# Kernel optimization log

Hardware: AMD Instinct MI355X
Metric: run time of the kernel (lower is better)

Reference implementation:

```python
import jax, jax.numpy as jnp
import numpy as np

IN_CAPS, IN_SIZE = 2401, 8
OUT_CAPS, OUT_SIZE = 8, 16
ROUTING_ITERS = 3


def squash(s, axis):
    mag_sq = jnp.sum(s * s, axis=axis, keepdims=True)
    mag = jnp.sqrt(mag_sq)
    return mag_sq / (1.0 + mag_sq) * (s / mag)


def setup_inputs() -> dict:
    key = jax.random.key(0)
    kx, kw = jax.random.split(key)
    B = 256
    x = jax.random.normal(kx, (B, IN_CAPS, IN_SIZE), dtype=jnp.float32)
    stdv = 1.0 / np.sqrt(IN_CAPS)
    W = jax.random.uniform(kw, (IN_CAPS, OUT_CAPS, OUT_SIZE, IN_SIZE),
                           dtype=jnp.float32, minval=-stdv, maxval=stdv)
    return {"x": x, "W": W}


def reference(x, W):
    # u_hat[b,i,o,c] = W[i,o,c,d] @ x[b,i,d]   -> [B, 2401, 8, 16]
    u_hat = jnp.einsum('iocd,bid->bioc', W, x)
    u_hat_det = jax.lax.stop_gradient(u_hat)

    b_ij = jnp.zeros((IN_CAPS, OUT_CAPS), dtype=x.dtype)
    v_j = None
    for it in range(ROUTING_ITERS):
        c_ij = jax.nn.softmax(b_ij, axis=1)  # softmax over out_capsules
        last = (it == ROUTING_ITERS - 1)
        u = u_hat if last else u_hat_det
        s_j = jnp.einsum('io,bioc->boc', c_ij, u)  # [B, 8, 16]
        v_j = squash(s_j, axis=-1)
        if not last:
            # agreement: mean over batch of <u_hat_i, v_j>
            a = jnp.einsum('bioc,boc->io', u_hat_det, v_j) / x.shape[0]
            b_ij = b_ij + a
    return v_j  # [B, 8, 16]
```

## Files before the change

kernel.cpp:

```cpp
#include <hip/hip_runtime.h>
#include <math.h>

#define IC     2401
#define BSZ    256
#define OC     8
#define CS     16
#define OCC    128
#define XROW   19208
#define KP     19264
#define KTILES 301
#define NI     64

typedef __attribute__((ext_vector_type(8))) short short8;
typedef __attribute__((ext_vector_type(4))) float f32x4;

__device__ __forceinline__ unsigned short f2bf(float f) {
    union { float f; unsigned u; } v; v.f = f;
    const unsigned r = v.u + 0x7FFF + ((v.u >> 16) & 1);
    return (unsigned short)(r >> 16);
}
__device__ __forceinline__ float bf2f(unsigned short h) {
    union { unsigned u; float f; } v; v.u = ((unsigned)h) << 16;
    return v.f;
}

__global__ __launch_bounds__(256)
void prep_kernel(const float* __restrict__ x, const float* __restrict__ W,
                 unsigned short* __restrict__ xT, unsigned short* __restrict__ xB,
                 unsigned short* __restrict__ Wbf, unsigned short* __restrict__ cwt)
{
    const int tid = threadIdx.x;
    if (blockIdx.x < 1204) {
        __shared__ float Ts[64 * 65];
        const int bg = blockIdx.x & 3;
        const int kt = blockIdx.x >> 2;
#pragma unroll
        for (int r = 0; r < 4; ++r) {
            const int flat = r * 256 + tid;
            const int b = flat >> 4, cq = flat & 15;
            const int col = kt * 64 + cq * 4;
            float4 v = make_float4(0.f, 0.f, 0.f, 0.f);
            if (col < XROW) v = *(const float4*)(x + (size_t)(bg * 64 + b) * XROW + col);
            *(float4*)&Ts[b * 65 + cq * 4] = v;
        }
        __syncthreads();
#pragma unroll
        for (int r = 0; r < 2; ++r) {
            const int flat = r * 256 + tid;
            const int rl = flat >> 3, bq = flat & 7;
            union { short8 v; unsigned short h[8]; } o;
#pragma unroll
            for (int j = 0; j < 8; ++j) o.h[j] = f2bf(Ts[(bq * 8 + j) * 65 + rl]);
            *(short8*)(xT + (size_t)(kt * 64 + rl) * 256 + bg * 64 + bq * 8) = o.v;
        }
#pragma unroll
        for (int r = 0; r < 2; ++r) {
            const int flat = r * 256 + tid;
            const int b = flat >> 3, g = flat & 7;
            union { short8 v; unsigned short h[8]; } o;
#pragma unroll
            for (int j = 0; j < 8; ++j) o.h[j] = f2bf(Ts[b * 65 + g * 8 + j]);
            *(short8*)(xB + (size_t)(bg * 64 + b) * KP + (size_t)kt * 64 + g * 8) = o.v;
        }
    } else {
        __shared__ float Ws[8 * 1032];
        const int i0 = (blockIdx.x - 1204) * 8;
#pragma unroll
        for (int r = 0; r < 8; ++r) {
            const int flat = r * 256 + tid;
            const int g = flat >> 8, rem = flat & 255;
            int gi = i0 + g; if (gi > 2400) gi = 2400;
            const float4 v = *(const float4*)(W + (size_t)gi * 1024 + rem * 4);
            *(float4*)&Ws[g * 1032 + rem * 4] = v;
        }
        __syncthreads();
#pragma unroll
        for (int r = 0; r < 4; ++r) {
            const int flat = r * 256 + tid;
            const int oc = flat >> 3, g = flat & 7;
            const int gi = i0 + g;
            union { short8 v; unsigned short h[8]; } w, c;
            if (gi <= 2400) {
                const float* wp = &Ws[g * 1032 + oc * 8];
#pragma unroll
                for (int j = 0; j < 8; ++j) {
                    w.h[j] = f2bf(wp[j]);
                    c.h[j] = f2bf(0.125f * wp[j]);
                }
            } else {
#pragma unroll
                for (int j = 0; j < 8; ++j) { w.h[j] = 0; c.h[j] = 0; }
            }
            *(short8*)(Wbf + (size_t)oc * KP + (size_t)gi * 8) = w.v;
            *(short8*)(cwt + (size_t)oc * KP + (size_t)gi * 8) = c.v;
        }
    }
}

__global__ __launch_bounds__(256, 2)
void s_gemm(const unsigned short* __restrict__ xB, const unsigned short* __restrict__ cwt,
            float* __restrict__ spart)
{
    __shared__ __align__(16) unsigned short Xs[64 * 64];
    __shared__ __align__(16) unsigned short Bs[128 * 64];
    const int tid = threadIdx.x;
    const int bg  = blockIdx.x, iy = blockIdx.y;
    const int b0  = bg * 64;
    const int ln  = tid & 63;
    const int mr  = ln & 15, qd = ln >> 4;
    const int mh  = (tid >> 6) & 1;
    const int nh  = tid >> 7;

    f32x4 acc[2][4];
#pragma unroll
    for (int a = 0; a < 2; ++a)
#pragma unroll
        for (int b = 0; b < 4; ++b) acc[a][b] = (f32x4){0.f, 0.f, 0.f, 0.f};

    for (int kt = iy; kt < KTILES; kt += NI) {
        __syncthreads();
#pragma unroll
        for (int r = 0; r < 2; ++r) {
            const int flat = r * 256 + tid;
            const int b = flat >> 3, col = flat & 7;
            const short8 v = *(const short8*)(xB + (size_t)(b0 + b) * KP + (size_t)(kt * 8 + col) * 8);
            *(short8*)&Xs[b * 64 + ((col ^ (b & 7)) * 8)] = v;
        }
#pragma unroll
        for (int r = 0; r < 4; ++r) {
            const int flat = r * 256 + tid;
            const int oc = flat >> 3, col = flat & 7;
            const short8 w = *(const short8*)(cwt + (size_t)oc * KP + (size_t)(kt * 8 + col) * 8);
            *(short8*)&Bs[oc * 64 + ((col ^ (oc & 7)) * 8)] = w;
        }
        __syncthreads();
#pragma unroll
        for (int kk = 0; kk < 2; ++kk) {
            const int csw = ((kk * 4 + qd) ^ (mr & 7)) * 8;
            const short8 a0 = *(const short8*)&Xs[(mh * 32 + mr) * 64 + csw];
            const short8 a1 = *(const short8*)&Xs[(mh * 32 + 16 + mr) * 64 + csw];
#pragma unroll
            for (int nt = 0; nt < 4; ++nt) {
                const short8 b = *(const short8*)&Bs[(nh * 64 + nt * 16 + mr) * 64 + csw];
                acc[0][nt] = __builtin_amdgcn_mfma_f32_16x16x32_bf16(a0, b, acc[0][nt], 0, 0, 0);
                acc[1][nt] = __builtin_amdgcn_mfma_f32_16x16x32_bf16(a1, b, acc[1][nt], 0, 0, 0);
            }
        }
    }

    float* op = spart + ((size_t)iy * BSZ + b0) * OCC;
#pragma unroll
    for (int mt = 0; mt < 2; ++mt)
#pragma unroll
        for (int nt = 0; nt < 4; ++nt)
#pragma unroll
            for (int r = 0; r < 4; ++r)
                op[(size_t)(mh * 32 + mt * 16 + qd * 4 + r) * OCC + nh * 64 + nt * 16 + mr]
                    = acc[mt][nt][r];
}

__global__ __launch_bounds__(256)
void squash_kernel(const float* __restrict__ spart, float* __restrict__ vout,
                   unsigned short* __restrict__ vT, int writeT)
{
    __shared__ float red[256];
    const int tid = threadIdx.x;
    const int r0  = blockIdx.x * 8;
    const int idx = tid & 127;
    const int k0  = tid >> 7;

    const float* base = spart + (size_t)r0 * 16 + idx;
    float acc = 0.0f;
#pragma unroll 8
    for (int k = k0; k < NI; k += 2) acc += base[(size_t)k * (BSZ * OCC)];
    red[tid] = acc;
    __syncthreads();

    if (tid < 128) {
        const float s = red[tid] + red[tid + 128];
        float ms = s * s;
        ms += __shfl_xor(ms, 1); ms += __shfl_xor(ms, 2);
        ms += __shfl_xor(ms, 4); ms += __shfl_xor(ms, 8);
        const float scale = sqrtf(ms) / (1.0f + ms);
        const float outv = s * scale;
        const int row = r0 + (tid >> 4);
        const int j   = tid & 15;
        if (writeT) {
            vT[(size_t)((row & 7) * 16 + j) * 256 + (row >> 3)] = f2bf(outv);
        } else {
            vout[(size_t)row * 16 + j] = outv;
        }
    }
}

template<bool FIRST>
__global__ __launch_bounds__(256, 2)
void a_gemm(const unsigned short* __restrict__ xT, const unsigned short* __restrict__ vT,
            const unsigned short* __restrict__ Wbf, float* __restrict__ bij,
            unsigned short* __restrict__ cwt)
{
    __shared__ __align__(16) char smraw[128 * 68 * 4];
    unsigned short* As = (unsigned short*)smraw;
    unsigned short* Bx = (unsigned short*)(smraw + 16384);
    float* Hs = (float*)smraw;

    const int tid = threadIdx.x;
    const int i0  = blockIdx.x * 8;
    const int ln  = tid & 63, wv = tid >> 6;
    const int mr  = ln & 15, qd = ln >> 4;

    f32x4 acc[2][4];
#pragma unroll
    for (int a = 0; a < 2; ++a)
#pragma unroll
        for (int b = 0; b < 4; ++b) acc[a][b] = (f32x4){0.f, 0.f, 0.f, 0.f};

    for (int bc = 0; bc < 4; ++bc) {
        __syncthreads();
#pragma unroll
        for (int r = 0; r < 4; ++r) {
            const int flat = r * 256 + tid;
            const int oc = flat >> 3, col = flat & 7;
            const short8 v = *(const short8*)(vT + (size_t)oc * 256 + bc * 64 + col * 8);
            *(short8*)&As[oc * 64 + ((col ^ (oc & 7)) * 8)] = v;
        }
#pragma unroll
        for (int r = 0; r < 2; ++r) {
            const int flat = r * 256 + tid;
            const int rw = flat >> 3, col = flat & 7;
            const short8 v = *(const short8*)(xT + (size_t)(i0 * 8 + rw) * 256 + bc * 64 + col * 8);
            *(short8*)&Bx[rw * 64 + ((col ^ (rw & 7)) * 8)] = v;
        }
        __syncthreads();
#pragma unroll
        for (int kk = 0; kk < 2; ++kk) {
            const int csw = ((kk * 4 + qd) ^ (mr & 7)) * 8;
#pragma unroll
            for (int nt = 0; nt < 4; ++nt) {
                const short8 b = *(const short8*)&Bx[(nt * 16 + mr) * 64 + csw];
#pragma unroll
                for (int mt = 0; mt < 2; ++mt) {
                    const short8 a = *(const short8*)&As[((wv * 2 + mt) * 16 + mr) * 64 + csw];
                    acc[mt][nt] = __builtin_amdgcn_mfma_f32_16x16x32_bf16(a, b, acc[mt][nt], 0, 0, 0);
                }
            }
        }
    }

    __syncthreads();
#pragma unroll
    for (int mt = 0; mt < 2; ++mt)
#pragma unroll
        for (int nt = 0; nt < 4; ++nt)
#pragma unroll
            for (int r = 0; r < 4; ++r)
                Hs[((wv * 2 + mt) * 16 + qd * 4 + r) * 68 + nt * 16 + mr] = acc[mt][nt][r];
    __syncthreads();

    const int ch = tid & 3, oo = (tid >> 2) & 7, il = tid >> 5;
    const int ival = i0 + il;
    const int gi = (ival < IC) ? ival : IC - 1;
    const unsigned short* Wt = Wbf + (size_t)(oo * 16 + ch * 4) * KP + (size_t)gi * 8;

    float wreg[4][8];
#pragma unroll
    for (int c = 0; c < 4; ++c) {
        union { short8 v; unsigned short h[8]; } uw;
        uw.v = *(const short8*)(Wt + (size_t)c * KP);
#pragma unroll
        for (int j = 0; j < 8; ++j) wreg[c][j] = bf2f(uw.h[j]);
    }
    float p = 0.0f;
#pragma unroll
    for (int c = 0; c < 4; ++c) {
        const float* hr = &Hs[(oo * 16 + ch * 4 + c) * 68 + il * 8];
        const float4 h0 = *(const float4*)hr;
        const float4 h1 = *(const float4*)(hr + 4);
        p = fmaf(wreg[c][0], h0.x, p); p = fmaf(wreg[c][1], h0.y, p);
        p = fmaf(wreg[c][2], h0.z, p); p = fmaf(wreg[c][3], h0.w, p);
        p = fmaf(wreg[c][4], h1.x, p); p = fmaf(wreg[c][5], h1.y, p);
        p = fmaf(wreg[c][6], h1.z, p); p = fmaf(wreg[c][7], h1.w, p);
    }
    p += __shfl_xor(p, 1); p += __shfl_xor(p, 2);
    const float anew = p * (1.0f / 256.0f);
    float bv = anew;
    if (!FIRST) bv += bij[gi * 8 + oo];
    float mx = bv;
    mx = fmaxf(mx, __shfl_xor(mx, 4));
    mx = fmaxf(mx, __shfl_xor(mx, 8));
    mx = fmaxf(mx, __shfl_xor(mx, 16));
    const float e = expf(bv - mx);
    float ss = e;
    ss += __shfl_xor(ss, 4); ss += __shfl_xor(ss, 8); ss += __shfl_xor(ss, 16);
    float cv = e / ss;
    if (ival >= IC) cv = 0.0f;
    if (ch == 0 && ival < IC) bij[ival * 8 + oo] = bv;
#pragma unroll
    for (int c = 0; c < 4; ++c) {
        union { short8 v; unsigned short h[8]; } o;
#pragma unroll
        for (int j = 0; j < 8; ++j) o.h[j] = f2bf(cv * wreg[c][j]);
        *(short8*)(cwt + (size_t)(oo * 16 + ch * 4 + c) * KP + (size_t)ival * 8) = o.v;
    }
}

extern "C" void kernel_launch(void* const* d_in, const int* in_sizes, int n_in,
                              void* d_out, int out_size, void* d_ws, size_t ws_size,
                              hipStream_t stream)
{
    const float* x = (const float*)d_in[0];
    const float* W = (const float*)d_in[1];
    float* out = (float*)d_out;

    char* p = (char*)d_ws;
    float*          spart = (float*)p;          p += (size_t)NI * BSZ * OCC * 4;
    unsigned short* xT    = (unsigned short*)p; p += (size_t)KP * 256 * 2;
    unsigned short* xB    = (unsigned short*)p; p += (size_t)256 * KP * 2;
    unsigned short* Wbf   = (unsigned short*)p; p += (size_t)128 * KP * 2;
    unsigned short* cwt   = (unsigned short*)p; p += (size_t)128 * KP * 2;
    unsigned short* vT    = (unsigned short*)p; p += (size_t)128 * 256 * 2;
    float*          bij   = (float*)p;

    const dim3 sgrid(4, NI);

    prep_kernel<<<1505, 256, 0, stream>>>(x, W, xT, xB, Wbf, cwt);

    s_gemm<<<sgrid, 256, 0, stream>>>(xB, cwt, spart);
    squash_kernel<<<256, 256, 0, stream>>>(spart, nullptr, vT, 1);
    a_gemm<true><<<KTILES, 256, 0, stream>>>(xT, vT, Wbf, bij, cwt);
    s_gemm<<<sgrid, 256, 0, stream>>>(xB, cwt, spart);
    squash_kernel<<<256, 256, 0, stream>>>(spart, nullptr, vT, 1);
    a_gemm<false><<<KTILES, 256, 0, stream>>>(xT, vT, Wbf, bij, cwt);
    s_gemm<<<sgrid, 256, 0, stream>>>(xB, cwt, spart);
    squash_kernel<<<256, 256, 0, stream>>>(spart, out, vT, 0);
}
```

Baseline: 142.4 us.

## Fuse routing iterations into one persistent cooperative kernel with grid syncs

Replaces the eight separate s_gemm/squash/a_gemm launches with a single cooperative kernel of 256 blocks that runs all routing phases and separates them with grid-wide syncs. This is meant to remove per-launch overhead and the gaps between dependent kernels. In exchange, the a_gemm phase now runs with 256 blocks looping over 301 tiles, so a few blocks do two tiles. Occupancy also drops to one block per CU, and every grid.sync has its own cost. If the cooperative launch fails, the code falls back to separate launches.

Result: slower. 380.9 us (+167.4%).

```diff
diff --git a/kernel.cpp b/kernel.cpp
--- a/kernel.cpp
+++ b/kernel.cpp
@@ -1,5 +1,8 @@
 #include <hip/hip_runtime.h>
+#include <hip/hip_cooperative_groups.h>
 #include <math.h>
+
+namespace cg = cooperative_groups;
 
 #define IC     2401
 #define BSZ    256
@@ -97,19 +100,18 @@
     }
 }
 
-__global__ __launch_bounds__(256, 2)
-void s_gemm(const unsigned short* __restrict__ xB, const unsigned short* __restrict__ cwt,
-            float* __restrict__ spart)
-{
-    __shared__ __align__(16) unsigned short Xs[64 * 64];
-    __shared__ __align__(16) unsigned short Bs[128 * 64];
-    const int tid = threadIdx.x;
-    const int bg  = blockIdx.x, iy = blockIdx.y;
-    const int b0  = bg * 64;
-    const int ln  = tid & 63;
-    const int mr  = ln & 15, qd = ln >> 4;
-    const int mh  = (tid >> 6) & 1;
-    const int nh  = tid >> 7;
+__device__ __forceinline__ void s_phase(char* smraw, const int tid, const int bid,
+        const unsigned short* __restrict__ xB, const unsigned short* __restrict__ cwt,
+        float* __restrict__ spart)
+{
+    unsigned short* Xs = (unsigned short*)smraw;
+    unsigned short* Bs = (unsigned short*)(smraw + 8192);
+    const int bg = bid & 3, iy = bid >> 2;
+    const int b0 = bg * 64;
+    const int ln = tid & 63;
+    const int mr = ln & 15, qd = ln >> 4;
+    const int mh = (tid >> 6) & 1;
+    const int nh = tid >> 7;
 
     f32x4 acc[2][4];
 #pragma unroll
@@ -159,13 +161,11 @@
                     = acc[mt][nt][r];
 }
 
-__global__ __launch_bounds__(256)
-void squash_kernel(const float* __restrict__ spart, float* __restrict__ vout,
-                   unsigned short* __restrict__ vT, int writeT)
-{
-    __shared__ float red[256];
-    const int tid = threadIdx.x;
-    const int r0  = blockIdx.x * 8;
+__device__ __forceinline__ void q_phase(char* smraw, const int tid, const int bid, const int writeT,
+        const float* __restrict__ spart, float* __restrict__ vout, unsigned short* __restrict__ vT)
+{
+    float* red = (float*)smraw;
+    const int r0  = bid * 8;
     const int idx = tid & 127;
     const int k0  = tid >> 7;
 
@@ -193,19 +193,16 @@
     }
 }
 
-template<bool FIRST>
-__global__ __launch_bounds__(256, 2)
-void a_gemm(const unsigned short* __restrict__ xT, const unsigned short* __restrict__ vT,
-            const unsigned short* __restrict__ Wbf, float* __restrict__ bij,
-            unsigned short* __restrict__ cwt)
-{
-    __shared__ __align__(16) char smraw[128 * 68 * 4];
+__device__ __forceinline__ void a_phase(char* smraw, const int tid, const int t, const int first,
+        const unsigned short* __restrict__ xT, const unsigned short* __restrict__ vT,
+        const unsigned short* __restrict__ Wbf, float* __restrict__ bij,
+        unsigned short* __restrict__ cwt)
+{
     unsigned short* As = (unsigned short*)smraw;
     unsigned short* Bx = (unsigned short*)(smraw + 16384);
     float* Hs = (float*)smraw;
 
-    const int tid = threadIdx.x;
-    const int i0  = blockIdx.x * 8;
+    const int i0  = t * 8;
     const int ln  = tid & 63, wv = tid >> 6;
     const int mr  = ln & 15, qd = ln >> 4;
 
@@ -284,7 +281,7 @@
     p += __shfl_xor(p, 1); p += __shfl_xor(p, 2);
     const float anew = p * (1.0f / 256.0f);
     float bv = anew;
-    if (!FIRST) bv += bij[gi * 8 + oo];
+    if (!first) bv += bij[gi * 8 + oo];
     float mx = bv;
     mx = fmaxf(mx, __shfl_xor(mx, 4));
     mx = fmaxf(mx, __shfl_xor(mx, 8));
@@ -304,6 +301,60 @@
     }
 }
 
+__global__ __launch_bounds__(256, 1)
+void routing_kernel(const unsigned short* __restrict__ xT,
+                    const unsigned short* __restrict__ xB,
+                    const unsigned short* __restrict__ Wbf,
+                    unsigned short* __restrict__ cwt,
+                    float* __restrict__ spart,
+                    unsigned short* __restrict__ vT,
+                    float* __restrict__ bij,
+                    float* __restrict__ out)
+{
+    cg::grid_group grid = cg::this_grid();
+    __shared__ __align__(16) char sm[128 * 68 * 4];
+    const int tid = threadIdx.x;
+    const int bid = blockIdx.x;
+
+#pragma unroll 1
+    for (int iter = 0; iter < 3; ++iter) {
+        s_phase(sm, tid, bid, xB, cwt, spart);
+        grid.sync();
+        q_phase(sm, tid, bid, (iter < 2) ? 1 : 0, spart, out, vT);
+        if (iter == 2) return;
+        grid.sync();
+        for (int t = bid; t < KTILES; t += 256)
+            a_phase(sm, tid, t, (iter == 0) ? 1 : 0, xT, vT, Wbf, bij, cwt);
+        grid.sync();
+    }
+}
+
+__global__ __launch_bounds__(256, 2)
+void s_gemm_k(const unsigned short* __restrict__ xB, const unsigned short* __restrict__ cwt,
+              float* __restrict__ spart)
+{
+    __shared__ __align__(16) char sm[24576];
+    s_phase(sm, threadIdx.x, blockIdx.x, xB, cwt, spart);
+}
+
+__global__ __launch_bounds__(256)
+void squash_k(const float* __restrict__ spart, float* __restrict__ vout,
+              unsigned short* __restrict__ vT, int writeT)
+{
+    __shared__ __align__(16) char sm[1024];
+    q_phase(sm, threadIdx.x, blockIdx.x, writeT, spart, vout, vT);
+}
+
+__global__ __launch_bounds__(256, 2)
+void a_gemm_k(const unsigned short* __restrict__ xT, const unsigned short* __restrict__ vT,
+              const unsigned short* __restrict__ Wbf, float* __restrict__ bij,
+              unsigned short* __restrict__ cwt, int first)
+{
+    __shared__ __align__(16) char sm[34816];
+    for (int t = blockIdx.x; t < KTILES; t += gridDim.x)
+        a_phase(sm, threadIdx.x, t, first, xT, vT, Wbf, bij, cwt);
+}
+
 extern "C" void kernel_launch(void* const* d_in, const int* in_sizes, int n_in,
                               void* d_out, int out_size, void* d_ws, size_t ws_size,
                               hipStream_t stream)
@@ -321,16 +372,20 @@
     unsigned short* vT    = (unsigned short*)p; p += (size_t)128 * 256 * 2;
     float*          bij   = (float*)p;
 
-    const dim3 sgrid(4, NI);
-
     prep_kernel<<<1505, 256, 0, stream>>>(x, W, xT, xB, Wbf, cwt);
 
-    s_gemm<<<sgrid, 256, 0, stream>>>(xB, cwt, spart);
-    squash_kernel<<<256, 256, 0, stream>>>(spart, nullptr, vT, 1);
-    a_gemm<true><<<KTILES, 256, 0, stream>>>(xT, vT, Wbf, bij, cwt);
-    s_gemm<<<sgrid, 256, 0, stream>>>(xB, cwt, spart);
-    squash_kernel<<<256, 256, 0, stream>>>(spart, nullptr, vT, 1);
-    a_gemm<false><<<KTILES, 256, 0, stream>>>(xT, vT, Wbf, bij, cwt);
-    s_gemm<<<sgrid, 256, 0, stream>>>(xB, cwt, spart);
-    squash_kernel<<<256, 256, 0, stream>>>(spart, out, vT, 0);
-}
+    void* kargs[] = { (void*)&xT, (void*)&xB, (void*)&Wbf, (void*)&cwt,
+                      (void*)&spart, (void*)&vT, (void*)&bij, (void*)&out };
+    hipError_t err = hipLaunchCooperativeKernel((void*)routing_kernel,
+                                                dim3(256), dim3(256), kargs, 0, stream);
+    if (err != hipSuccess) {
+        s_gemm_k<<<256, 256, 0, stream>>>(xB, cwt, spart);
+        squash_k<<<256, 256, 0, stream>>>(spart, nullptr, vT, 1);
+        a_gemm_k<<<256, 256, 0, stream>>>(xT, vT, Wbf, bij, cwt, 1);
+        s_gemm_k<<<256, 256, 0, stream>>>(xB, cwt, spart);
+        squash_k<<<256, 256, 0, stream>>>(spart, nullptr, vT, 1);
+        a_gemm_k<<<256, 256, 0, stream>>>(xT, vT, Wbf, bij, cwt, 0);
+        s_gemm_k<<<256, 256, 0, stream>>>(xB, cwt, spart);
+        squash_k<<<256, 256, 0, stream>>>(spart, out, vT, 0);
+    }
+}
```

## Register-prefetch next K tile in both MFMA GEMMs and double split-K partitions

Applied to the files above, without the earlier changes.

Both MFMA GEMM kernels now load the next tile's global data into registers before computing on the current shared-memory tile. This overlaps global-load latency with the MFMA work. The split-K factor NI also doubles from 64 to 128, giving more blocks for parallelism. The cost is more partial sums for the squash/reduce kernel to read and some extra register pressure.

Result: no change. 141.3 us (-0.8%).

```diff
diff --git a/kernel.cpp b/kernel.cpp
--- a/kernel.cpp
+++ b/kernel.cpp
@@ -9,7 +9,7 @@
 #define XROW   19208
 #define KP     19264
 #define KTILES 301
-#define NI     64
+#define NI     128
 
 typedef __attribute__((ext_vector_type(8))) short short8;
 typedef __attribute__((ext_vector_type(4))) float f32x4;
@@ -117,21 +117,30 @@
 #pragma unroll
         for (int b = 0; b < 4; ++b) acc[a][b] = (f32x4){0.f, 0.f, 0.f, 0.f};
 
-    for (int kt = iy; kt < KTILES; kt += NI) {
-        __syncthreads();
-#pragma unroll
-        for (int r = 0; r < 2; ++r) {
-            const int flat = r * 256 + tid;
-            const int b = flat >> 3, col = flat & 7;
-            const short8 v = *(const short8*)(xB + (size_t)(b0 + b) * KP + (size_t)(kt * 8 + col) * 8);
-            *(short8*)&Xs[b * 64 + ((col ^ (b & 7)) * 8)] = v;
-        }
-#pragma unroll
-        for (int r = 0; r < 4; ++r) {
-            const int flat = r * 256 + tid;
-            const int oc = flat >> 3, col = flat & 7;
-            const short8 w = *(const short8*)(cwt + (size_t)oc * KP + (size_t)(kt * 8 + col) * 8);
-            *(short8*)&Bs[oc * 64 + ((col ^ (oc & 7)) * 8)] = w;
+    const int srow = tid >> 3, scol = tid & 7;
+    const int ssw  = (scol ^ (srow & 7)) * 8;
+    const unsigned short* xp0 = xB  + (size_t)(b0 + srow) * KP + (size_t)scol * 8;
+    const unsigned short* bp0 = cwt + (size_t)srow * KP + (size_t)scol * 8;
+
+    short8 vx[2], vb[4];
+    int kt = iy;
+#pragma unroll
+    for (int r = 0; r < 2; ++r) vx[r] = *(const short8*)(xp0 + (size_t)r * 32 * KP + (size_t)kt * 64);
+#pragma unroll
+    for (int r = 0; r < 4; ++r) vb[r] = *(const short8*)(bp0 + (size_t)r * 32 * KP + (size_t)kt * 64);
+
+    while (true) {
+        __syncthreads();
+#pragma unroll
+        for (int r = 0; r < 2; ++r) *(short8*)&Xs[(r * 32 + srow) * 64 + ssw] = vx[r];
+#pragma unroll
+        for (int r = 0; r < 4; ++r) *(short8*)&Bs[(r * 32 + srow) * 64 + ssw] = vb[r];
+        const int ktn = kt + NI;
+        if (ktn < KTILES) {
+#pragma unroll
+            for (int r = 0; r < 2; ++r) vx[r] = *(const short8*)(xp0 + (size_t)r * 32 * KP + (size_t)ktn * 64);
+#pragma unroll
+            for (int r = 0; r < 4; ++r) vb[r] = *(const short8*)(bp0 + (size_t)r * 32 * KP + (size_t)ktn * 64);
         }
         __syncthreads();
 #pragma unroll
@@ -146,6 +155,8 @@
                 acc[1][nt] = __builtin_amdgcn_mfma_f32_16x16x32_bf16(a1, b, acc[1][nt], 0, 0, 0);
             }
         }
+        if (ktn >= KTILES) break;
+        kt = ktn;
     }
 
     float* op = spart + ((size_t)iy * BSZ + b0) * OCC;
@@ -215,21 +226,28 @@
 #pragma unroll
         for (int b = 0; b < 4; ++b) acc[a][b] = (f32x4){0.f, 0.f, 0.f, 0.f};
 
+    const int srow = tid >> 3, scol = tid & 7;
+    const int ssw  = (scol ^ (srow & 7)) * 8;
+    const unsigned short* ap0 = vT + (size_t)srow * 256 + (size_t)scol * 8;
+    const unsigned short* bp0 = xT + (size_t)(i0 * 8 + srow) * 256 + (size_t)scol * 8;
+
+    short8 va[4], vbx[2];
+#pragma unroll
+    for (int r = 0; r < 4; ++r) va[r]  = *(const short8*)(ap0 + (size_t)r * 32 * 256);
+#pragma unroll
+    for (int r = 0; r < 2; ++r) vbx[r] = *(const short8*)(bp0 + (size_t)r * 32 * 256);
+
     for (int bc = 0; bc < 4; ++bc) {
         __syncthreads();
 #pragma unroll
-        for (int r = 0; r < 4; ++r) {
-            const int flat = r * 256 + tid;
-            const int oc = flat >> 3, col = flat & 7;
-            const short8 v = *(const short8*)(vT + (size_t)oc * 256 + bc * 64 + col * 8);
-            *(short8*)&As[oc * 64 + ((col ^ (oc & 7)) * 8)] = v;
-        }
-#pragma unroll
-        for (int r = 0; r < 2; ++r) {
-            const int flat = r * 256 + tid;
-            const int rw = flat >> 3, col = flat & 7;
-            const short8 v = *(const short8*)(xT + (size_t)(i0 * 8 + rw) * 256 + bc * 64 + col * 8);
-            *(short8*)&Bx[rw * 64 + ((col ^ (rw & 7)) * 8)] = v;
+        for (int r = 0; r < 4; ++r) *(short8*)&As[(r * 32 + srow) * 64 + ssw] = va[r];
+#pragma unroll
+        for (int r = 0; r < 2; ++r) *(short8*)&Bx[(r * 32 + srow) * 64 + ssw] = vbx[r];
+        if (bc < 3) {
+#pragma unroll
+            for (int r = 0; r < 4; ++r) va[r]  = *(const short8*)(ap0 + (size_t)r * 32 * 256 + (bc + 1) * 64);
+#pragma unroll
+            for (int r = 0; r < 2; ++r) vbx[r] = *(const short8*)(bp0 + (size_t)r * 32 * 256 + (bc + 1) * 64);
         }
         __syncthreads();
 #pragma unroll
```
